# Kernel tuning notes

Measured on AMD Instinct MI355X. Metric: run time of the kernel, lower is better.

The kernel has to match this reference:

```python
import math
import jax, jax.numpy as jnp
import numpy as np

B, N, F, FE = 16, 24, 128, 128   # crystals, atoms/crystal, atom feat, edge feat
NUM_Z = 100                       # num_atomic_numbers
GAUSS_STOP, BASIS_W = 6.0, 1.0
RADIUS_RATE = 1.0
N_CONV, N_FC, FC_F = 3, 4, 128
REP = 1                           # PBC replication per axis (27 images); exact for our cells
ZDIM = 2 * F + FE


def setup_inputs() -> dict:
    key = jax.random.key(0)
    ks = jax.random.split(key, 12)
    # cubic cells with side length in [8, 10) Angstrom -> rep per axis is exactly 1
    L = 8.0 + 2.0 * jax.random.uniform(ks[0], (B,))
    cell = L[:, None, None] * jnp.eye(3, dtype=jnp.float32)          # [B,3,3]
    frac = jax.random.uniform(ks[1], (B, N, 3))
    pos = jnp.einsum('bnd,bde->bne', frac, cell).reshape(B * N, 3)   # [B*N,3]
    atomic_numbers = jax.random.randint(ks[2], (B * N,), 1, NUM_Z + 1)
    batch = jnp.repeat(jnp.arange(B), N)
    emb = jax.random.normal(ks[3], (NUM_Z, F)) * 0.1                 # embedding table
    s = 1.0 / math.sqrt(ZDIM)
    conv_Wf = jax.random.normal(ks[4], (N_CONV, ZDIM, F)) * s
    conv_bf = jnp.zeros((N_CONV, F))
    conv_Ws = jax.random.normal(ks[5], (N_CONV, ZDIM, F)) * s
    conv_bs = jnp.zeros((N_CONV, F))
    sf = 1.0 / math.sqrt(FC_F)
    fc_W = jax.random.normal(ks[6], (N_FC - 1, FC_F, FC_F)) * sf
    fc_b = jnp.zeros((N_FC - 1, FC_F))
    W_out = jax.random.normal(ks[7], (FC_F, 1)) * sf
    b_out = jnp.zeros((1,))
    return {'pos': pos, 'cell': cell, 'emb': emb,
            'conv_Wf': conv_Wf, 'conv_bf': conv_bf,
            'conv_Ws': conv_Ws, 'conv_bs': conv_bs,
            'fc_W': fc_W, 'fc_b': fc_b, 'W_out': W_out, 'b_out': b_out,
            'atomic_numbers': atomic_numbers, 'batch': batch}


def _spectral_normalize(W, iters=5, eps=1e-12):
    # power iteration; sigma differentiable through W only (u,v detached) as in torch
    u = jnp.ones((W.shape[1],), W.dtype)
    u = u / jnp.linalg.norm(u)
    for _ in range(iters):
        v = W @ u
        v = v / (jnp.linalg.norm(v) + eps)
        u = W.T @ v
        u = u / (jnp.linalg.norm(u) + eps)
    u = jax.lax.stop_gradient(u)
    v = jax.lax.stop_gradient(v)
    sigma = v @ (W @ u)
    return W / sigma


def _forward(pos, cell, emb, conv_Wf, conv_bf, conv_Ws, conv_bs,
             fc_W, fc_b, W_out, b_out, atomic_numbers):
    # ---- graph construction (PBC all-pairs, fixed 27 images, masked) ----
    r = jnp.arange(-REP, REP + 1, dtype=cell.dtype)
    grid = jnp.stack(jnp.meshgrid(r, r, r, indexing='ij'), -1).reshape(-1, 3)  # [27,3]
    pbc = jnp.einsum('cd,bde->bce', grid, cell)                                # [B,27,3]
    posb = pos.reshape(B, N, 3)
    # disp[b,i,j,c] = pos_i - (pos_j + offset_c)
    disp = posb[:, :, None, None, :] - (posb[:, None, :, None, :] + pbc[:, None, None, :, :])
    dsqr = jnp.sum(disp * disp, -1)                                            # [B,N,N,27]
    cross = jnp.cross(cell[:, 1], cell[:, 2])
    vol = jnp.sum(cell[:, 0] * cross, -1)
    radius = RADIUS_RATE * (jnp.abs(vol) / N) ** (1.0 / 3.0)                   # [B]
    rb = radius[:, None, None, None]
    mask = (dsqr <= rb * rb) & (dsqr > 1e-4)
    dist = jnp.sqrt(jnp.maximum(dsqr, 1e-12))
    mf = mask.astype(pos.dtype)
    edge_w = (jnp.cos(dist * math.pi / rb) + 1.0) * mf                         # [B,N,N,27]
    # GaussianSmearing
    goff = jnp.linspace(0.0, GAUSS_STOP, FE)
    coeff = -0.5 / (BASIS_W * (goff[1] - goff[0])) ** 2
    edge_attr = jnp.exp(coeff * (dist[..., None] - goff) ** 2)                 # [B,N,N,27,FE]

    # ---- node features ----
    feat = jnp.tanh(emb[atomic_numbers - 1]).reshape(B, N, F)

    # ---- continuous graph convs (CGCNN-style gated conv, edge_weight scaled) ----
    for l in range(N_CONV):
        Wf, Ws = conv_Wf[l], conv_Ws[l]
        gi = feat @ Wf[:F]; gj = feat @ Wf[F:2 * F]
        ge = jnp.einsum('bijce,ef->bijcf', edge_attr, Wf[2 * F:])
        g = jax.nn.sigmoid(gi[:, :, None, None, :] + gj[:, None, :, None, :] + ge + conv_bf[l])
        si = feat @ Ws[:F]; sj = feat @ Ws[F:2 * F]
        se = jnp.einsum('bijce,ef->bijcf', edge_attr, Ws[2 * F:])
        sc = jax.nn.softplus(si[:, :, None, None, :] + sj[:, None, :, None, :] + se + conv_bs[l])
        msg = g * sc * edge_w[..., None]                                       # [B,N,N,27,F]
        feat = jax.nn.softplus(feat + msg.sum((2, 3)))                         # aggregate at i

    # ---- global mean pool + spectral-norm MLP head ----
    h = feat.mean(1)                                                           # [B,F]
    for l in range(N_FC - 1):
        h = jax.nn.softplus(h @ _spectral_normalize(fc_W[l]) + fc_b[l])
    return h @ W_out + b_out                                                   # [B,1]


def reference(pos, cell, emb, conv_Wf, conv_bf, conv_Ws, conv_bs,
              fc_W, fc_b, W_out, b_out, atomic_numbers, batch):
    return _forward(pos, cell, emb, conv_Wf, conv_bf, conv_Ws, conv_bs,
                    fc_W, fc_b, W_out, b_out, atomic_numbers)
```

## Files before the change

kernel.cpp:

```cpp
#include <hip/hip_runtime.h>
#include <math.h>

#define NB 16
#define NN 24
#define NA 384
#define FF 128
#define CC 27
#define MAXNBR 32

__device__ int   g_cnt[NA];
__device__ float g_sigma[4];
__device__ int   g_nj[NA*MAXNBR];
__device__ float g_nd[NA*MAXNBR];
__device__ float g_nw[NA*MAXNBR];
__device__ float g_featA[NA*FF];
__device__ float g_featB[NA*FF];
__device__ float g_projA[NA*4*FF];
__device__ float g_projB[NA*4*FF];
__device__ float g_feat [NA*FF];
__device__ int   g_arrive[NB];

__device__ __forceinline__ float softplusf(float x){ return fmaxf(x,0.f) + log1pf(expf(-fabsf(x))); }
__device__ __forceinline__ float sigmoidf(float x){ return 1.f/(1.f+expf(-x)); }
__device__ __forceinline__ void st_agent(float* p, float v){
  __hip_atomic_store(p, v, __ATOMIC_RELAXED, __HIP_MEMORY_SCOPE_AGENT);
}
__device__ __forceinline__ float ld_agent(const float* p){
  return __hip_atomic_load(p, __ATOMIC_RELAXED, __HIP_MEMORY_SCOPE_AGENT);
}

__global__ void __launch_bounds__(512)
k_prep(const float* __restrict__ pos, const float* __restrict__ cell,
       const float* __restrict__ emb, const float* __restrict__ fc_W,
       const float* __restrict__ conv_Wf, const float* __restrict__ conv_Ws,
       const int* __restrict__ z)
{
  const int bid = blockIdx.x, tid = threadIdx.x;
  const int q = tid >> 7, f = tid & 127;

  if (bid < 3) {
    __shared__ float s_w[FF*129];
    __shared__ float s_u[FF], s_v[FF], s_red[FF];
    __shared__ float s_part[4][FF];
    const float* W = fc_W + bid*FF*FF;
    for (int idx = tid; idx < FF*FF; idx += 512)
      s_w[(idx >> 7)*129 + (idx & 127)] = W[idx];
    if (tid < FF) s_u[tid] = 0.08838834764831845f;
    __syncthreads();
    for (int it = 0; it < 5; it++) {
      { float p = 0.f;
        #pragma unroll
        for (int k = q*32; k < q*32+32; k++) p += s_w[f*129+k]*s_u[k];
        s_part[q][f] = p; }
      __syncthreads();
      if (tid < FF) { float s = s_part[0][f]+s_part[1][f]+s_part[2][f]+s_part[3][f];
                      s_v[f] = s; s_red[f] = s*s; }
      __syncthreads();
      for (int st=64; st>0; st>>=1){ if (tid<st) s_red[tid]+=s_red[tid+st]; __syncthreads(); }
      float nv = sqrtf(s_red[0]) + 1e-12f;
      __syncthreads();
      if (tid < FF) s_v[f] /= nv;
      __syncthreads();
      { float p = 0.f;
        #pragma unroll
        for (int r = q*32; r < q*32+32; r++) p += s_w[r*129+f]*s_v[r];
        s_part[q][f] = p; }
      __syncthreads();
      if (tid < FF) { float s = s_part[0][f]+s_part[1][f]+s_part[2][f]+s_part[3][f];
                      s_u[f] = s; s_red[f] = s*s; }
      __syncthreads();
      for (int st=64; st>0; st>>=1){ if (tid<st) s_red[tid]+=s_red[tid+st]; __syncthreads(); }
      float nu = sqrtf(s_red[0]) + 1e-12f;
      __syncthreads();
      if (tid < FF) s_u[f] /= nu;
      __syncthreads();
    }
    { float p = 0.f;
      #pragma unroll
      for (int k = q*32; k < q*32+32; k++) p += s_w[f*129+k]*s_u[k];
      s_part[q][f] = p; }
    __syncthreads();
    if (tid < FF) s_red[f] = s_v[f]*(s_part[0][f]+s_part[1][f]+s_part[2][f]+s_part[3][f]);
    __syncthreads();
    for (int st=64; st>0; st>>=1){ if (tid<st) s_red[tid]+=s_red[tid+st]; __syncthreads(); }
    if (tid == 0) g_sigma[bid] = s_red[0];
  } else {
    const int i = bid - 3;
    const int b = i / NN;
    __shared__ float ft[FF];
    __shared__ float s_cell[9];
    __shared__ float s_rb;
    __shared__ int   s_cnt;
    if (tid < FF) {
      int zi = z[i]; if (zi < 1) zi = 1; if (zi > 100) zi = 100;
      float v = tanhf(emb[(zi-1)*FF+tid]);
      ft[tid] = v;
      g_featA[i*FF+tid] = v;
    }
    if (tid >= 256 && tid < 265) s_cell[tid-256] = cell[b*9 + tid - 256];
    if (tid == 500) s_cnt = 0;
    __syncthreads();
    if (tid == 0) {
      const float* c = s_cell;
      float cx = c[4]*c[8] - c[5]*c[7];
      float cy = c[5]*c[6] - c[3]*c[8];
      float cz = c[3]*c[7] - c[4]*c[6];
      float vol = c[0]*cx + c[1]*cy + c[2]*cz;
      s_rb = cbrtf(fabsf(vol)/(float)NN);
    }
    __syncthreads();
    const float rb = s_rb, rb2 = rb*rb;
    const float pix = pos[i*3+0], piy = pos[i*3+1], piz = pos[i*3+2];
    const float PI = 3.14159265358979323846f;
    for (int cand = tid; cand < NN*CC; cand += 512) {
      int j = cand / CC, c = cand - j*CC;
      float gx = (float)(c/9) - 1.0f;
      float gy = (float)((c/3)%3) - 1.0f;
      float gz = (float)(c%3) - 1.0f;
      float ox = gx*s_cell[0] + gy*s_cell[3] + gz*s_cell[6];
      float oy = gx*s_cell[1] + gy*s_cell[4] + gz*s_cell[7];
      float oz = gx*s_cell[2] + gy*s_cell[5] + gz*s_cell[8];
      int jg = b*NN + j;
      float dx = pix - (pos[jg*3+0] + ox);
      float dy = piy - (pos[jg*3+1] + oy);
      float dz = piz - (pos[jg*3+2] + oz);
      float d2 = dx*dx + dy*dy + dz*dz;
      if (d2 <= rb2 && d2 > 1e-4f) {
        float dist = sqrtf(fmaxf(d2, 1e-12f));
        float w = cosf(dist*PI/rb) + 1.0f;
        int slot = atomicAdd(&s_cnt, 1);
        if (slot < MAXNBR) {
          g_nj[i*MAXNBR+slot] = jg;
          g_nd[i*MAXNBR+slot] = dist;
          g_nw[i*MAXNBR+slot] = w;
        }
      }
    }
    __syncthreads();
    if (tid == 0) g_cnt[i] = (s_cnt > MAXNBR) ? MAXNBR : s_cnt;
    const float* W = (q==0) ? conv_Wf
                   : (q==1) ? (conv_Wf + FF*FF)
                   : (q==2) ? conv_Ws
                   :          (conv_Ws + FF*FF);
    float s = 0.f;
    #pragma unroll 8
    for (int k=0;k<FF;k++) s += ft[k]*W[k*FF+f];
    g_projA[(i*4+q)*FF+f] = s;
  }
}

template<int LAYER>
__global__ void __launch_bounds__(512)
k_edge(const float* __restrict__ conv_Wf, const float* __restrict__ conv_bf,
       const float* __restrict__ conv_Ws, const float* __restrict__ conv_bs)
{
  const int i = blockIdx.x, tid = threadIdx.x;
  const int q = tid >> 7, f = tid & 127;
  const float* projSrc = (LAYER==0) ? g_projA : g_projB;
  float*       projDst = (LAYER==0) ? g_projB : g_projA;
  const float* fin  = (LAYER==0) ? g_featA : g_featB;
  float*       fout = (LAYER==0) ? g_featB : g_featA;
  const float* Wf2 = conv_Wf + LAYER*3*FF*FF + 2*FF*FF;
  const float* Ws2 = conv_Ws + LAYER*3*FF*FF + 2*FF*FF;

  const float gi  = projSrc[(i*4+0)*FF+f];
  const float si  = projSrc[(i*4+2)*FF+f];
  const float bff = conv_bf[LAYER*FF+f];
  const float bsf = conv_bs[LAYER*FF+f];
  const float step  = 6.0f/127.0f;
  const float coeff = -0.5f/(step*step);
  const int n = g_cnt[i];

  float msg = 0.f;
  for (int e = q; e < n; e += 4) {
    const int   jg   = g_nj[i*MAXNBR+e];
    const float dist = g_nd[i*MAXNBR+e];
    const float w    = g_nw[i*MAXNBR+e];
    const float gj   = projSrc[(jg*4+1)*FF+f];
    const float sj   = projSrc[(jg*4+3)*FF+f];
    float center = dist / step;
    int kmin = (int)ceilf(center - 9.0f);  if (kmin < 0)   kmin = 0;
    int kmax = (int)floorf(center + 9.0f); if (kmax > 127) kmax = 127;
    float ge = 0.f, se = 0.f;
    for (int k = kmin; k <= kmax; k++) {
      float dd = dist - step*(float)k;
      float a  = expf(coeff*dd*dd);
      ge += a * Wf2[k*FF+f];
      se += a * Ws2[k*FF+f];
    }
    msg += sigmoidf(gi + gj + ge + bff) * softplusf(si + sj + se + bsf) * w;
  }

  __shared__ float sm[4][FF];
  __shared__ float fnew[FF];
  sm[q][f] = msg;
  __syncthreads();
  if (tid < FF) {
    float v = softplusf(fin[i*FF+f] + sm[0][f] + sm[1][f] + sm[2][f] + sm[3][f]);
    fnew[f] = v;
    fout[i*FF+f] = v;
  }
  __syncthreads();
  const float* WfN = conv_Wf + (LAYER+1)*3*FF*FF;
  const float* WsN = conv_Ws + (LAYER+1)*3*FF*FF;
  const float* W = (q==0) ? WfN : (q==1) ? (WfN + FF*FF) : (q==2) ? WsN : (WsN + FF*FF);
  float s = 0.f;
  #pragma unroll 8
  for (int k=0;k<FF;k++) s += fnew[k]*W[k*FF+f];
  projDst[(i*4+q)*FF+f] = s;
}

__global__ void __launch_bounds__(512)
k_edge2f(const float* __restrict__ conv_Wf, const float* __restrict__ conv_bf,
         const float* __restrict__ conv_Ws, const float* __restrict__ conv_bs,
         const float* __restrict__ fc_W,  const float* __restrict__ fc_b,
         const float* __restrict__ W_out, const float* __restrict__ b_out,
         float* __restrict__ out)
{
  const int i = blockIdx.x, tid = threadIdx.x;
  const int q = tid >> 7, f = tid & 127;
  const int b = i / NN;
  const float* Wf2 = conv_Wf + 2*3*FF*FF + 2*FF*FF;
  const float* Ws2 = conv_Ws + 2*3*FF*FF + 2*FF*FF;

  const float gi  = g_projA[(i*4+0)*FF+f];
  const float si  = g_projA[(i*4+2)*FF+f];
  const float bff = conv_bf[2*FF+f];
  const float bsf = conv_bs[2*FF+f];
  const float step  = 6.0f/127.0f;
  const float coeff = -0.5f/(step*step);
  const int n = g_cnt[i];

  float msg = 0.f;
  for (int e = q; e < n; e += 4) {
    const int   jg   = g_nj[i*MAXNBR+e];
    const float dist = g_nd[i*MAXNBR+e];
    const float w    = g_nw[i*MAXNBR+e];
    const float gj   = g_projA[(jg*4+1)*FF+f];
    const float sj   = g_projA[(jg*4+3)*FF+f];
    float center = dist / step;
    int kmin = (int)ceilf(center - 9.0f);  if (kmin < 0)   kmin = 0;
    int kmax = (int)floorf(center + 9.0f); if (kmax > 127) kmax = 127;
    float ge = 0.f, se = 0.f;
    for (int k = kmin; k <= kmax; k++) {
      float dd = dist - step*(float)k;
      float a  = expf(coeff*dd*dd);
      ge += a * Wf2[k*FF+f];
      se += a * Ws2[k*FF+f];
    }
    msg += sigmoidf(gi + gj + ge + bff) * softplusf(si + sj + se + bsf) * w;
  }

  __shared__ float sm[4][FF];
  __shared__ int   s_old;
  sm[q][f] = msg;
  __syncthreads();
  if (tid < FF) {
    float v = softplusf(g_featB[i*FF+f] + sm[0][f] + sm[1][f] + sm[2][f] + sm[3][f]);
    st_agent(&g_feat[i*FF+f], v);
  }
  asm volatile("s_waitcnt vmcnt(0)" ::: "memory");
  __syncthreads();
  if (tid == 0)
    s_old = __hip_atomic_fetch_add(&g_arrive[b], 1, __ATOMIC_ACQ_REL,
                                   __HIP_MEMORY_SCOPE_AGENT);
  __syncthreads();
  if (s_old != NN-1) return;

  __shared__ float s_hh[FF], s_tmp[FF], s_part[4][FF], s_red[FF];
  if (tid < FF) {
    float s0 = 0.f;
    for (int a = 0; a < NN; a++) s0 += ld_agent(&g_feat[(b*NN+a)*FF+tid]);
    s_hh[tid] = s0/(float)NN;
  }
  __syncthreads();
  for (int l = 0; l < 3; l++) {
    { float p = 0.f;
      #pragma unroll
      for (int k = q*32; k < q*32+32; k++) p += s_hh[k]*fc_W[l*FF*FF + k*FF + f];
      s_part[q][f] = p; }
    __syncthreads();
    if (tid < FF) {
      float s = s_part[0][tid]+s_part[1][tid]+s_part[2][tid]+s_part[3][tid];
      s_tmp[tid] = softplusf(s/g_sigma[l] + fc_b[l*FF+tid]);
    }
    __syncthreads();
    if (tid < FF) s_hh[tid] = s_tmp[tid];
    __syncthreads();
  }
  if (tid < FF) s_red[tid] = s_hh[tid]*W_out[tid];
  __syncthreads();
  if (tid < 64) {
    float t = s_red[tid] + s_red[tid+64];
    #pragma unroll
    for (int off = 32; off > 0; off >>= 1) t += __shfl_xor(t, off);
    if (tid == 0) {
      out[b] = t + b_out[0];
      __hip_atomic_store(&g_arrive[b], 0, __ATOMIC_RELAXED,
                         __HIP_MEMORY_SCOPE_AGENT);
    }
  }
}

extern "C" void kernel_launch(void* const* d_in, const int* in_sizes, int n_in,
                              void* d_out, int out_size, void* d_ws, size_t ws_size,
                              hipStream_t stream) {
  const float* pos     = (const float*)d_in[0];
  const float* cell    = (const float*)d_in[1];
  const float* emb     = (const float*)d_in[2];
  const float* conv_Wf = (const float*)d_in[3];
  const float* conv_bf = (const float*)d_in[4];
  const float* conv_Ws = (const float*)d_in[5];
  const float* conv_bs = (const float*)d_in[6];
  const float* fc_W    = (const float*)d_in[7];
  const float* fc_b    = (const float*)d_in[8];
  const float* W_out   = (const float*)d_in[9];
  const float* b_out   = (const float*)d_in[10];
  const int*   z       = (const int*)d_in[11];

  k_prep   <<<NA+3, 512, 0, stream>>>(pos, cell, emb, fc_W, conv_Wf, conv_Ws, z);
  k_edge<0><<<NA,   512, 0, stream>>>(conv_Wf, conv_bf, conv_Ws, conv_bs);
  k_edge<1><<<NA,   512, 0, stream>>>(conv_Wf, conv_bf, conv_Ws, conv_bs);
  k_edge2f <<<NA,   512, 0, stream>>>(conv_Wf, conv_bf, conv_Ws, conv_bs,
                                      fc_W, fc_b, W_out, b_out, (float*)d_out);
}
```

Before: 144.7 us.

## Fuse last two conv layers into one kernel with per-crystal spin barrier

Merges conv layers 2 and 3 and the readout head into a single kernel. A per-crystal atomic counter with a spin-wait replaces the kernel boundary between the layers, so one launch and its global drain disappear. The spin barrier assumes all 384 blocks are co-resident, which risks deadlock if occupancy drops. It also adds spin latency while blocks wait for the rest of their crystal.

```diff
diff --git a/kernel.cpp b/kernel.cpp
--- a/kernel.cpp
+++ b/kernel.cpp
@@ -18,7 +18,8 @@
 __device__ float g_projA[NA*4*FF];
 __device__ float g_projB[NA*4*FF];
 __device__ float g_feat [NA*FF];
-__device__ int   g_arrive[NB];
+__device__ int   g_arrE[NB];
+__device__ int   g_arrF[NB];
 
 __device__ __forceinline__ float softplusf(float x){ return fmaxf(x,0.f) + log1pf(expf(-fabsf(x))); }
 __device__ __forceinline__ float sigmoidf(float x){ return 1.f/(1.f+expf(-x)); }
@@ -149,84 +150,19 @@
   }
 }
 
-template<int LAYER>
 __global__ void __launch_bounds__(512)
-k_edge(const float* __restrict__ conv_Wf, const float* __restrict__ conv_bf,
-       const float* __restrict__ conv_Ws, const float* __restrict__ conv_bs)
+k_edge0(const float* __restrict__ conv_Wf, const float* __restrict__ conv_bf,
+        const float* __restrict__ conv_Ws, const float* __restrict__ conv_bs)
 {
   const int i = blockIdx.x, tid = threadIdx.x;
   const int q = tid >> 7, f = tid & 127;
-  const float* projSrc = (LAYER==0) ? g_projA : g_projB;
-  float*       projDst = (LAYER==0) ? g_projB : g_projA;
-  const float* fin  = (LAYER==0) ? g_featA : g_featB;
-  float*       fout = (LAYER==0) ? g_featB : g_featA;
-  const float* Wf2 = conv_Wf + LAYER*3*FF*FF + 2*FF*FF;
-  const float* Ws2 = conv_Ws + LAYER*3*FF*FF + 2*FF*FF;
-
-  const float gi  = projSrc[(i*4+0)*FF+f];
-  const float si  = projSrc[(i*4+2)*FF+f];
-  const float bff = conv_bf[LAYER*FF+f];
-  const float bsf = conv_bs[LAYER*FF+f];
-  const float step  = 6.0f/127.0f;
-  const float coeff = -0.5f/(step*step);
-  const int n = g_cnt[i];
-
-  float msg = 0.f;
-  for (int e = q; e < n; e += 4) {
-    const int   jg   = g_nj[i*MAXNBR+e];
-    const float dist = g_nd[i*MAXNBR+e];
-    const float w    = g_nw[i*MAXNBR+e];
-    const float gj   = projSrc[(jg*4+1)*FF+f];
-    const float sj   = projSrc[(jg*4+3)*FF+f];
-    float center = dist / step;
-    int kmin = (int)ceilf(center - 9.0f);  if (kmin < 0)   kmin = 0;
-    int kmax = (int)floorf(center + 9.0f); if (kmax > 127) kmax = 127;
-    float ge = 0.f, se = 0.f;
-    for (int k = kmin; k <= kmax; k++) {
-      float dd = dist - step*(float)k;
-      float a  = expf(coeff*dd*dd);
-      ge += a * Wf2[k*FF+f];
-      se += a * Ws2[k*FF+f];
-    }
-    msg += sigmoidf(gi + gj + ge + bff) * softplusf(si + sj + se + bsf) * w;
-  }
-
-  __shared__ float sm[4][FF];
-  __shared__ float fnew[FF];
-  sm[q][f] = msg;
-  __syncthreads();
-  if (tid < FF) {
-    float v = softplusf(fin[i*FF+f] + sm[0][f] + sm[1][f] + sm[2][f] + sm[3][f]);
-    fnew[f] = v;
-    fout[i*FF+f] = v;
-  }
-  __syncthreads();
-  const float* WfN = conv_Wf + (LAYER+1)*3*FF*FF;
-  const float* WsN = conv_Ws + (LAYER+1)*3*FF*FF;
-  const float* W = (q==0) ? WfN : (q==1) ? (WfN + FF*FF) : (q==2) ? WsN : (WsN + FF*FF);
-  float s = 0.f;
-  #pragma unroll 8
-  for (int k=0;k<FF;k++) s += fnew[k]*W[k*FF+f];
-  projDst[(i*4+q)*FF+f] = s;
-}
-
-__global__ void __launch_bounds__(512)
-k_edge2f(const float* __restrict__ conv_Wf, const float* __restrict__ conv_bf,
-         const float* __restrict__ conv_Ws, const float* __restrict__ conv_bs,
-         const float* __restrict__ fc_W,  const float* __restrict__ fc_b,
-         const float* __restrict__ W_out, const float* __restrict__ b_out,
-         float* __restrict__ out)
-{
-  const int i = blockIdx.x, tid = threadIdx.x;
-  const int q = tid >> 7, f = tid & 127;
-  const int b = i / NN;
-  const float* Wf2 = conv_Wf + 2*3*FF*FF + 2*FF*FF;
-  const float* Ws2 = conv_Ws + 2*3*FF*FF + 2*FF*FF;
+  const float* Wf2 = conv_Wf + 2*FF*FF;
+  const float* Ws2 = conv_Ws + 2*FF*FF;
 
   const float gi  = g_projA[(i*4+0)*FF+f];
   const float si  = g_projA[(i*4+2)*FF+f];
-  const float bff = conv_bf[2*FF+f];
-  const float bsf = conv_bs[2*FF+f];
+  const float bff = conv_bf[f];
+  const float bsf = conv_bs[f];
   const float step  = 6.0f/127.0f;
   const float coeff = -0.5f/(step*step);
   const int n = g_cnt[i];
@@ -252,17 +188,133 @@
   }
 
   __shared__ float sm[4][FF];
+  __shared__ float fnew[FF];
+  sm[q][f] = msg;
+  __syncthreads();
+  if (tid < FF) {
+    float v = softplusf(g_featA[i*FF+f] + sm[0][f] + sm[1][f] + sm[2][f] + sm[3][f]);
+    fnew[f] = v;
+    g_featB[i*FF+f] = v;
+  }
+  __syncthreads();
+  const float* WfN = conv_Wf + 3*FF*FF;
+  const float* WsN = conv_Ws + 3*FF*FF;
+  const float* W = (q==0) ? WfN : (q==1) ? (WfN + FF*FF) : (q==2) ? WsN : (WsN + FF*FF);
+  float s = 0.f;
+  #pragma unroll 8
+  for (int k=0;k<FF;k++) s += fnew[k]*W[k*FF+f];
+  g_projB[(i*4+q)*FF+f] = s;
+}
+
+__global__ void __launch_bounds__(512)
+k_tail(const float* __restrict__ conv_Wf, const float* __restrict__ conv_bf,
+       const float* __restrict__ conv_Ws, const float* __restrict__ conv_bs,
+       const float* __restrict__ fc_W,  const float* __restrict__ fc_b,
+       const float* __restrict__ W_out, const float* __restrict__ b_out,
+       float* __restrict__ out)
+{
+  const int i = blockIdx.x, tid = threadIdx.x;
+  const int q = tid >> 7, f = tid & 127;
+  const int b = i / NN;
+  const float step  = 6.0f/127.0f;
+  const float coeff = -0.5f/(step*step);
+  const int n = g_cnt[i];
+
+  __shared__ float sm[4][FF];
+  __shared__ float fnew[FF];
+  __shared__ float s_gi[FF], s_si[FF];
   __shared__ int   s_old;
-  sm[q][f] = msg;
-  __syncthreads();
-  if (tid < FF) {
-    float v = softplusf(g_featB[i*FF+f] + sm[0][f] + sm[1][f] + sm[2][f] + sm[3][f]);
-    st_agent(&g_feat[i*FF+f], v);
+
+  {
+    const float* Wf2 = conv_Wf + 1*3*FF*FF + 2*FF*FF;
+    const float* Ws2 = conv_Ws + 1*3*FF*FF + 2*FF*FF;
+    const float gi  = g_projB[(i*4+0)*FF+f];
+    const float si  = g_projB[(i*4+2)*FF+f];
+    const float bff = conv_bf[1*FF+f];
+    const float bsf = conv_bs[1*FF+f];
+    float msg = 0.f;
+    for (int e = q; e < n; e += 4) {
+      const int   jg   = g_nj[i*MAXNBR+e];
+      const float dist = g_nd[i*MAXNBR+e];
+      const float w    = g_nw[i*MAXNBR+e];
+      const float gj   = g_projB[(jg*4+1)*FF+f];
+      const float sj   = g_projB[(jg*4+3)*FF+f];
+      float center = dist / step;
+      int kmin = (int)ceilf(center - 9.0f);  if (kmin < 0)   kmin = 0;
+      int kmax = (int)floorf(center + 9.0f); if (kmax > 127) kmax = 127;
+      float ge = 0.f, se = 0.f;
+      for (int k = kmin; k <= kmax; k++) {
+        float dd = dist - step*(float)k;
+        float a  = expf(coeff*dd*dd);
+        ge += a * Wf2[k*FF+f];
+        se += a * Ws2[k*FF+f];
+      }
+      msg += sigmoidf(gi + gj + ge + bff) * softplusf(si + sj + se + bsf) * w;
+    }
+    sm[q][f] = msg;
+    __syncthreads();
+    if (tid < FF)
+      fnew[f] = softplusf(g_featB[i*FF+f] + sm[0][f]+sm[1][f]+sm[2][f]+sm[3][f]);
+    __syncthreads();
+  }
+
+  {
+    const float* WfN = conv_Wf + 2*3*FF*FF;
+    const float* WsN = conv_Ws + 2*3*FF*FF;
+    const float* W = (q==0) ? WfN : (q==1) ? (WfN+FF*FF) : (q==2) ? WsN : (WsN+FF*FF);
+    float s = 0.f;
+    #pragma unroll 8
+    for (int k=0;k<FF;k++) s += fnew[k]*W[k*FF+f];
+    if (q==0) s_gi[f] = s;
+    if (q==2) s_si[f] = s;
+    st_agent(&g_projA[(i*4+q)*FF+f], s);
   }
   asm volatile("s_waitcnt vmcnt(0)" ::: "memory");
   __syncthreads();
+  if (tid == 0) {
+    __hip_atomic_fetch_add(&g_arrE[b], 1, __ATOMIC_ACQ_REL, __HIP_MEMORY_SCOPE_AGENT);
+    while (__hip_atomic_load(&g_arrE[b], __ATOMIC_ACQUIRE, __HIP_MEMORY_SCOPE_AGENT) < NN)
+      __builtin_amdgcn_s_sleep(2);
+  }
+  __syncthreads();
+
+  {
+    const float* Wf2 = conv_Wf + 2*3*FF*FF + 2*FF*FF;
+    const float* Ws2 = conv_Ws + 2*3*FF*FF + 2*FF*FF;
+    const float gi  = s_gi[f];
+    const float si  = s_si[f];
+    const float bff = conv_bf[2*FF+f];
+    const float bsf = conv_bs[2*FF+f];
+    float msg = 0.f;
+    for (int e = q; e < n; e += 4) {
+      const int   jg   = g_nj[i*MAXNBR+e];
+      const float dist = g_nd[i*MAXNBR+e];
+      const float w    = g_nw[i*MAXNBR+e];
+      const float gj   = ld_agent(&g_projA[(jg*4+1)*FF+f]);
+      const float sj   = ld_agent(&g_projA[(jg*4+3)*FF+f]);
+      float center = dist / step;
+      int kmin = (int)ceilf(center - 9.0f);  if (kmin < 0)   kmin = 0;
+      int kmax = (int)floorf(center + 9.0f); if (kmax > 127) kmax = 127;
+      float ge = 0.f, se = 0.f;
+      for (int k = kmin; k <= kmax; k++) {
+        float dd = dist - step*(float)k;
+        float a  = expf(coeff*dd*dd);
+        ge += a * Wf2[k*FF+f];
+        se += a * Ws2[k*FF+f];
+      }
+      msg += sigmoidf(gi + gj + ge + bff) * softplusf(si + sj + se + bsf) * w;
+    }
+    sm[q][f] = msg;
+    __syncthreads();
+    if (tid < FF) {
+      float v = softplusf(fnew[f] + sm[0][f]+sm[1][f]+sm[2][f]+sm[3][f]);
+      st_agent(&g_feat[i*FF+f], v);
+    }
+  }
+  asm volatile("s_waitcnt vmcnt(0)" ::: "memory");
+  __syncthreads();
   if (tid == 0)
-    s_old = __hip_atomic_fetch_add(&g_arrive[b], 1, __ATOMIC_ACQ_REL,
+    s_old = __hip_atomic_fetch_add(&g_arrF[b], 1, __ATOMIC_ACQ_REL,
                                    __HIP_MEMORY_SCOPE_AGENT);
   __syncthreads();
   if (s_old != NN-1) return;
@@ -296,8 +348,8 @@
     for (int off = 32; off > 0; off >>= 1) t += __shfl_xor(t, off);
     if (tid == 0) {
       out[b] = t + b_out[0];
-      __hip_atomic_store(&g_arrive[b], 0, __ATOMIC_RELAXED,
-                         __HIP_MEMORY_SCOPE_AGENT);
+      __hip_atomic_store(&g_arrE[b], 0, __ATOMIC_RELAXED, __HIP_MEMORY_SCOPE_AGENT);
+      __hip_atomic_store(&g_arrF[b], 0, __ATOMIC_RELAXED, __HIP_MEMORY_SCOPE_AGENT);
     }
   }
 }
@@ -318,9 +370,8 @@
   const float* b_out   = (const float*)d_in[10];
   const int*   z       = (const int*)d_in[11];
 
-  k_prep   <<<NA+3, 512, 0, stream>>>(pos, cell, emb, fc_W, conv_Wf, conv_Ws, z);
-  k_edge<0><<<NA,   512, 0, stream>>>(conv_Wf, conv_bf, conv_Ws, conv_bs);
-  k_edge<1><<<NA,   512, 0, stream>>>(conv_Wf, conv_bf, conv_Ws, conv_bs);
-  k_edge2f <<<NA,   512, 0, stream>>>(conv_Wf, conv_bf, conv_Ws, conv_bs,
-                                      fc_W, fc_b, W_out, b_out, (float*)d_out);
-}
+  k_prep <<<NA+3, 512, 0, stream>>>(pos, cell, emb, fc_W, conv_Wf, conv_Ws, z);
+  k_edge0<<<NA,   512, 0, stream>>>(conv_Wf, conv_bf, conv_Ws, conv_bs);
+  k_tail <<<NA,   512, 0, stream>>>(conv_Wf, conv_bf, conv_Ws, conv_bs,
+                                    fc_W, fc_b, W_out, b_out, (float*)d_out);
+}
```

New measurement: 211.2 us. 1.46x slower.
